# Performance work log

Measured on AMD Instinct MI355X. Metric: run time of the kernel, lower is better.

The kernel has to match this reference:

```python
import jax, jax.numpy as jnp
import numpy as np

M, N, T = 32, 32, 512
H1 = (M + N) * 10 * 8      # 5120
H2 = M * N * 4             # 4096
HID = 1000                 # GRU hidden (hardcoded in module)
EPS = 1e-12


def _l2norm(x):
    # torch.nn.functional.normalize: x / max(||x||_2, eps)
    return x / jnp.maximum(jnp.linalg.norm(x), EPS)


def setup_inputs() -> dict:
    key = jax.random.key(0)
    ks = jax.random.split(key, 16)
    rn = lambda k, shp, s: (jax.random.normal(k, shp, dtype=jnp.float32) * s)
    inp = {
        "y": rn(ks[0], (T, N), 1.0),
        "F": rn(ks[1], (M, M), 0.5 / np.sqrt(M)),   # stable dynamics
        "H": rn(ks[2], (N, M), 1.0 / np.sqrt(M)),
        "m1x0": rn(ks[3], (M,), 1.0),
        "h0": rn(ks[4], (HID,), 1.0),
        "W1": rn(ks[5], (H1, M + N), 1.0 / np.sqrt(M + N)),
        "b1": rn(ks[6], (H1,), 0.01),
        "Wih": rn(ks[7], (3 * HID, H1), 1.0 / np.sqrt(H1)),
        "bih": rn(ks[8], (3 * HID,), 0.01),
        "Whh": rn(ks[9], (3 * HID, HID), 1.0 / np.sqrt(HID)),
        "bhh": rn(ks[10], (3 * HID,), 0.01),
        "W2": rn(ks[11], (H2, HID), 1.0 / np.sqrt(HID)),
        "b2": rn(ks[12], (H2,), 0.01),
        "W3": rn(ks[13], (M * N, H2), 1.0 / np.sqrt(H2)),
        "b3": rn(ks[14], (M * N,), 0.01),
    }
    return inp


def reference(y, F, H, m1x0, h0, W1, b1, Wih, bih, Whh, bhh, W2, b2, W3, b3):
    m, n = F.shape[0], H.shape[0]

    def step(carry, yt):
        m1x_prior, m1x_post, h = carry
        # step_prior
        m1x_prev_prior = m1x_prior
        m1x_prior = F @ m1x_post              # [m]
        m1y = H @ m1x_prior                   # [n]
        # step_KGain_est: features
        dm1x_n = _l2norm(m1x_post - m1x_prev_prior)
        dm1y_n = _l2norm(yt - m1y)
        kin = jnp.concatenate([dm1y_n, dm1x_n])  # [n+m]
        # KGain_step: Linear+ReLU -> single-step GRU -> Linear+ReLU -> Linear
        x = jax.nn.relu(W1 @ kin + b1)        # [H1]
        gi = Wih @ x + bih                    # [3*HID]
        gh = Whh @ h + bhh
        ir, iz, ic = jnp.split(gi, 3)
        hr, hz, hc = jnp.split(gh, 3)
        r = jax.nn.sigmoid(ir + hr)
        z = jax.nn.sigmoid(iz + hz)
        c = jnp.tanh(ic + r * hc)
        h_new = (1.0 - z) * c + z * h         # GRU hidden [HID]
        l2 = jax.nn.relu(W2 @ h_new + b2)     # [H2]
        KG = (W3 @ l2 + b3).reshape(m, n)     # Kalman gain
        # KNet_step: innovation update
        m1x_post_new = m1x_prior + KG @ (yt - m1y)
        return (m1x_prior, m1x_post_new, h_new), m1x_post_new

    init = (m1x0, m1x0, h0)
    _, posts = jax.lax.scan(step, init, y)
    return posts  # [T, m]
```

## Files before the change

kernel.cpp:

```cpp
#include <hip/hip_runtime.h>
#include <cmath>

#define Mdim 32
#define Ndim 32
#define Tsteps 512
#define H1dim 5120
#define H2dim 4096
#define HIDdim 1000
#define NWG 256
#define NTHR 1024
#define POLLER 320

typedef unsigned int u32;
typedef unsigned short u16;

__device__ u16 g_w2b[H2dim * HIDdim];
__device__ u16 g_w3t[H2dim * Mdim * Ndim];

#define OFF_WIH 0
#define OFF_WHH 122880
#define OFF_UNION 146880
#define OFF_H9 157120
#define OFF_MISC 161640
#define SMEM_BYTES 162560

#define MI_POST 0
#define MI_PRIOR 32
#define MI_INNOV 96
#define MI_KIN 128
#define MI_GI 192
#define MI_GH 204

__device__ __forceinline__ u16 f2bf(float f) {
  u32 u = __float_as_uint(f);
  return (u16)((u + 0x7fffu + ((u >> 16) & 1u)) >> 16);
}
__device__ __forceinline__ float bflo(u32 u) { return __uint_as_float(u << 16); }
__device__ __forceinline__ float bfhi(u32 u) { return __uint_as_float(u & 0xffff0000u); }

__device__ __forceinline__ float dot4(float4 a, float4 b) {
  return a.x * b.x + a.y * b.y + a.z * b.z + a.w * b.w;
}
__device__ __forceinline__ float dot8_bb(uint4 a, uint4 b) {
  float s = 0.f;
  s = fmaf(bflo(a.x), bflo(b.x), s); s = fmaf(bfhi(a.x), bfhi(b.x), s);
  s = fmaf(bflo(a.y), bflo(b.y), s); s = fmaf(bfhi(a.y), bfhi(b.y), s);
  s = fmaf(bflo(a.z), bflo(b.z), s); s = fmaf(bfhi(a.z), bfhi(b.z), s);
  s = fmaf(bflo(a.w), bflo(b.w), s); s = fmaf(bfhi(a.w), bfhi(b.w), s);
  return s;
}
__device__ __forceinline__ float dot8_bf(uint4 a, const float* x8) {
  float s = 0.f;
  s = fmaf(bflo(a.x), x8[0], s); s = fmaf(bfhi(a.x), x8[1], s);
  s = fmaf(bflo(a.y), x8[2], s); s = fmaf(bfhi(a.y), x8[3], s);
  s = fmaf(bflo(a.z), x8[4], s); s = fmaf(bfhi(a.z), x8[5], s);
  s = fmaf(bflo(a.w), x8[6], s); s = fmaf(bfhi(a.w), x8[7], s);
  return s;
}

__device__ __forceinline__ float wave_reduce64(float v) {
#pragma unroll
  for (int off = 32; off >= 1; off >>= 1) v += __shfl_xor(v, off, 64);
  return v;
}
__device__ __forceinline__ float group16_reduce(float v) {
#pragma unroll
  for (int off = 8; off >= 1; off >>= 1) v += __shfl_xor(v, off, 64);
  return v;
}

__device__ __forceinline__ float4 ldg_cg4(const float* p) {
  float4 r;
  asm volatile("global_load_dwordx4 %0, %1, off sc0 sc1\n\ts_waitcnt vmcnt(0)"
               : "=v"(r) : "v"(p) : "memory");
  return r;
}
__device__ __forceinline__ uint4 ldg_cg4u(const void* p) {
  uint4 r;
  asm volatile("global_load_dwordx4 %0, %1, off sc0 sc1\n\ts_waitcnt vmcnt(0)"
               : "=v"(r) : "v"(p) : "memory");
  return r;
}
__device__ __forceinline__ void ldg2_cg4(const float* p0, const float* p1,
                                         float4& r0, float4& r1) {
  asm volatile("global_load_dwordx4 %0, %2, off sc0 sc1\n\t"
               "global_load_dwordx4 %1, %3, off sc0 sc1\n\t"
               "s_waitcnt vmcnt(0)"
               : "=&v"(r0), "=&v"(r1) : "v"(p0), "v"(p1) : "memory");
}
__device__ __forceinline__ void stg_cg1(float* p, float v) {
  asm volatile("global_store_dword %0, %1, off sc0 sc1" :: "v"(p), "v"(v) : "memory");
}
__device__ __forceinline__ void stg_cg_u16(u16* p, u16 v) {
  u32 vv = v;
  asm volatile("global_store_short %0, %1, off sc0 sc1" :: "v"(p), "v"(vv) : "memory");
}

__device__ __forceinline__ void gb_arrive(u32* bar) {
  asm volatile("s_waitcnt vmcnt(0)" ::: "memory");
  __syncthreads();
  if (threadIdx.x == POLLER) {
    u32 g = (u32)blockIdx.x & 15u;
    u32 a = __hip_atomic_fetch_add(bar + g * 16, 1u, __ATOMIC_RELAXED,
                                   __HIP_MEMORY_SCOPE_AGENT);
    if ((a & 15u) == 15u) {
      u32 b = __hip_atomic_fetch_add(bar + 256, 1u, __ATOMIC_RELAXED,
                                     __HIP_MEMORY_SCOPE_AGENT);
      if ((b & 15u) == 15u)
        __hip_atomic_fetch_add(bar + 320, 1u, __ATOMIC_RELAXED,
                               __HIP_MEMORY_SCOPE_AGENT);
    }
  }
}
__device__ __forceinline__ void gb_wait(u32* bar, u32 nb) {
  if (threadIdx.x == POLLER) {
    while (__hip_atomic_load(bar + 320, __ATOMIC_RELAXED,
                             __HIP_MEMORY_SCOPE_AGENT) < nb)
      __builtin_amdgcn_s_sleep(2);
  }
  __syncthreads();
}

__global__ void convert_w2(const float* __restrict__ W2) {
  int i = blockIdx.x * 1024 + threadIdx.x;
  if (i < H2dim * HIDdim) g_w2b[i] = f2bf(W2[i]);
}

__global__ void convert_w3t(const float* __restrict__ W3) {
  __shared__ float tile[32][33];
  int tr = blockIdx.x >> 7;
  int tc = blockIdx.x & 127;
  int r0 = tr * 32, c0 = tc * 32;
  int j = threadIdx.x & 31, i0 = threadIdx.x >> 5;
#pragma unroll
  for (int p = 0; p < 4; ++p) {
    int i = i0 + p * 8;
    tile[i][j] = W3[(size_t)(r0 + i) * H2dim + c0 + j];
  }
  __syncthreads();
#pragma unroll
  for (int p = 0; p < 4; ++p) {
    int i = i0 + p * 8;
    g_w3t[(size_t)(c0 + i) * 1024 + r0 + j] = f2bf(tile[j][i]);
  }
}

__global__ void __launch_bounds__(NTHR, 4)
knet_kernel(const float* __restrict__ y, const float* __restrict__ F,
            const float* __restrict__ Hm, const float* __restrict__ m1x0,
            const float* __restrict__ h0, const float* __restrict__ W1,
            const float* __restrict__ b1, const float* __restrict__ Wih,
            const float* __restrict__ bih, const float* __restrict__ Whh,
            const float* __restrict__ bhh, const float* __restrict__ b2,
            const float* __restrict__ b3, float* __restrict__ out,
            u32* bar, u16* xb, float* hbuf, float* dpart) {
  extern __shared__ char smem[];
  u16* s_wih = (u16*)(smem + OFF_WIH);
  u16* s_whh = (u16*)(smem + OFF_WHH);
  u16* s_x = (u16*)(smem + OFF_UNION);
  float4* s_red4 = (float4*)(smem + OFF_UNION);
  float* s_redf = (float*)(smem + OFF_UNION);
  float* s_pd = (float*)(smem + OFF_UNION);
  float* s_h9 = (float*)(smem + OFF_H9);
  float* s_m = (float*)(smem + OFF_MISC);
  float* s_post = s_m + MI_POST;
  float* s_prior = s_m + MI_PRIOR;
  float* s_innov = s_m + MI_INNOV;
  float* s_kin = s_m + MI_KIN;
  float* s_gi = s_m + MI_GI;
  float* s_gh = s_m + MI_GH;

  const int tid = threadIdx.x;
  const int w = tid >> 6;
  const int lane = tid & 63;
  const int wg = blockIdx.x;
  const int k0 = wg * 4;
  const bool gru_wg = (wg < 250);
  u32 nb = 0;

  if (gru_wg) {
#pragma unroll 1
    for (int r = 0; r < 12; ++r) {
      const float* src = Wih + (size_t)((r >> 2) * HIDdim + k0 + (r & 3)) * H1dim;
      u16* dst = s_wih + r * H1dim;
      for (int e = tid; e < H1dim; e += NTHR) dst[e] = f2bf(src[e]);
    }
#pragma unroll 1
    for (int r = 0; r < 12; ++r) {
      const float* src = Whh + (size_t)((r >> 2) * HIDdim + k0 + (r & 3)) * HIDdim;
      u16* dst = s_whh + r * HIDdim;
      for (int e = tid; e < HIDdim; e += NTHR) dst[e] = f2bf(src[e]);
    }
  }
  if (tid < 250) {
    float4 hv = ((const float4*)h0)[tid];
    int b0 = tid * 4;
    s_h9[((b0 + 0) >> 3) * 9 + ((b0 + 0) & 7)] = hv.x;
    s_h9[((b0 + 1) >> 3) * 9 + ((b0 + 1) & 7)] = hv.y;
    s_h9[((b0 + 2) >> 3) * 9 + ((b0 + 2) & 7)] = hv.z;
    s_h9[((b0 + 3) >> 3) * 9 + ((b0 + 3) & 7)] = hv.w;
  }
  __syncthreads();

  const int c2 = wg * 16 + w;
  const uint4* w2p = (const uint4*)(g_w2b + (size_t)c2 * HIDdim);
  uint4 wr0r = w2p[lane];
  uint4 wr1r = make_uint4(0u, 0u, 0u, 0u);
  if (lane < 61) wr1r = w2p[lane + 64];
  const uint4* w3p = (const uint4*)(g_w3t + (size_t)c2 * 1024);
  uint4 t0r = w3p[2 * lane];
  uint4 t1r = w3p[2 * lane + 1];
  const float b2c = b2[c2];
  float4 w1c = make_float4(0.f, 0.f, 0.f, 0.f);
  float b1c = 0.f;
  int w1row = 0;
  if (w < 5) {
    w1row = wg * 20 + w * 4 + (lane >> 4);
    w1c = ((const float4*)W1)[w1row * 16 + (lane & 15)];
    b1c = b1[w1row];
  }
  float prior = 0.f, bb = 0.f, yv = 0.f;
  if (w == 0 && lane < 32) {
    prior = m1x0[lane];
    yv = y[lane];
  }

  auto gh_compute = [&]() {
    int base = (w - 12) * 3;
#pragma unroll
    for (int rr = 0; rr < 3; ++rr) {
      int r = base + rr;
      const uint4* wr = (const uint4*)(s_whh + r * HIDdim);
      float acc = dot8_bf(wr[lane], s_h9 + lane * 9);
      if (lane < 61) acc += dot8_bf(wr[lane + 64], s_h9 + (lane + 64) * 9);
      acc = wave_reduce64(acc);
      if (lane == 0) s_gh[r] = acc + bhh[(r >> 2) * HIDdim + k0 + (r & 3)];
    }
  };
  if (gru_wg && w >= 12) gh_compute();

  for (int t = 0; t < Tsteps; ++t) {
    if (t > 0) {
      float4 a0, a1;
      ldg2_cg4(dpart + tid * 4, dpart + (tid + 1024) * 4, a0, a1);
      float4 s;
      s.x = a0.x + a1.x; s.y = a0.y + a1.y; s.z = a0.z + a1.z; s.w = a0.w + a1.w;
#pragma unroll
      for (int off = 8; off <= 32; off <<= 1) {
        s.x += __shfl_xor(s.x, off, 64);
        s.y += __shfl_xor(s.y, off, 64);
        s.z += __shfl_xor(s.z, off, 64);
        s.w += __shfl_xor(s.w, off, 64);
      }
      if (lane < 8) s_red4[w * 8 + lane] = s;
    }
    __syncthreads();
    if (w == 0) {
      float p = 0.f, inn = 0.f;
      float prev = prior;
      if (lane < 32) {
        if (t == 0) {
          p = m1x0[lane];
        } else {
          float dsum = 0.f;
#pragma unroll
          for (int ww = 0; ww < 16; ++ww) dsum += s_redf[ww * 32 + lane];
          p = prior + dsum + bb;
          if (wg == 0) out[(t - 1) * Mdim + lane] = p;
        }
        s_post[lane] = p;
      }
      asm volatile("" ::: "memory");
      if (lane < 32) {
        const float4* Fr = (const float4*)(F + lane * Mdim);
        const float4* pp = (const float4*)s_post;
        float s = 0.f;
#pragma unroll
        for (int j = 0; j < 8; ++j) s += dot4(Fr[j], pp[j]);
        prior = s;
        s_prior[lane] = s;
      }
      asm volatile("" ::: "memory");
      if (lane < 32) {
        const float4* Hr = (const float4*)(Hm + lane * Mdim);
        const float4* pp = (const float4*)s_prior;
        float s = 0.f;
#pragma unroll
        for (int j = 0; j < 8; ++j) s += dot4(Hr[j], pp[j]);
        inn = yv - s;
        s_innov[lane] = inn;
      }
      float vd = __shfl(p, lane & 31, 64) - __shfl(prev, lane & 31, 64);
      float v = (lane < 32) ? inn : vd;
      float sq = v * v;
#pragma unroll
      for (int off = 16; off >= 1; off >>= 1) sq += __shfl_xor(sq, off, 32);
      s_kin[lane] = v / fmaxf(sqrtf(sq), 1e-12f);
    }
    __syncthreads();
    if (w < 5) {
      float s = dot4(w1c, ((const float4*)s_kin)[lane & 15]);
      s = group16_reduce(s);
      if ((lane & 15) == 0) stg_cg_u16(xb + w1row, f2bf(fmaxf(s + b1c, 0.f)));
    }
    ++nb;
    gb_arrive(bar);
    gb_wait(bar, nb);

    if (gru_wg) {
      if (tid < 640) ((uint4*)s_x)[tid] = ldg_cg4u((const char*)xb + tid * 16);
      __syncthreads();
      if (w < 12) {
        const uint4* wr = (const uint4*)(s_wih + w * H1dim);
        const uint4* xr = (const uint4*)s_x;
        float acc = 0.f;
#pragma unroll
        for (int i = 0; i < 10; ++i) {
          int j = lane + 64 * i;
          acc += dot8_bb(wr[j], xr[j]);
        }
        acc = wave_reduce64(acc);
        if (lane == 0) s_gi[w] = acc + bih[(w >> 2) * HIDdim + k0 + (w & 3)];
      }
      __syncthreads();
      if (tid < 4) {
        int k = k0 + tid;
        float hold = s_h9[(k >> 3) * 9 + (k & 7)];
        float ir = s_gi[tid], iz = s_gi[4 + tid], ic = s_gi[8 + tid];
        float r = 1.f / (1.f + expf(-(ir + s_gh[tid])));
        float z = 1.f / (1.f + expf(-(iz + s_gh[4 + tid])));
        float c_ = tanhf(ic + r * s_gh[8 + tid]);
        stg_cg1(hbuf + k, (1.f - z) * c_ + z * hold);
      }
    }
    ++nb;
    gb_arrive(bar);
    float u;
    {
      const float* iv = s_innov + 16 * (lane & 1);
      u = dot8_bf(t0r, iv) + dot8_bf(t1r, iv + 8);
      u += __shfl_xor(u, 1, 64);
    }
    gb_wait(bar, nb);

    if (tid < 250) {
      float4 hv = ldg_cg4(hbuf + tid * 4);
      int b0 = tid * 4;
      s_h9[((b0 + 0) >> 3) * 9 + ((b0 + 0) & 7)] = hv.x;
      s_h9[((b0 + 1) >> 3) * 9 + ((b0 + 1) & 7)] = hv.y;
      s_h9[((b0 + 2) >> 3) * 9 + ((b0 + 2) & 7)] = hv.z;
      s_h9[((b0 + 3) >> 3) * 9 + ((b0 + 3) & 7)] = hv.w;
    }
    __syncthreads();
    {
      float acc = dot8_bf(wr0r, s_h9 + lane * 9);
      if (lane < 61) acc += dot8_bf(wr1r, s_h9 + (lane + 64) * 9);
      acc = wave_reduce64(acc);
      float l2c = fmaxf(acc + b2c, 0.f);
      if ((lane & 1) == 0) s_pd[w * 32 + (lane >> 1)] = l2c * u;
    }
    __syncthreads();
    if (tid < 32) {
      float pdv = 0.f;
#pragma unroll
      for (int ww = 0; ww < 16; ++ww) pdv += s_pd[ww * 32 + tid];
      stg_cg1(dpart + wg * 32 + tid, pdv);
    }
    ++nb;
    gb_arrive(bar);
    if (gru_wg && w >= 12) gh_compute();
    if (w == 0 && lane < 32) {
      int tn = (t + 1 < Tsteps) ? t + 1 : Tsteps - 1;
      yv = y[tn * Ndim + lane];
      float b = 0.f;
#pragma unroll 8
      for (int j = 0; j < 32; ++j) b = fmaf(b3[lane * 32 + j], s_innov[j], b);
      bb = b;
    }
    gb_wait(bar, nb);
  }

  if (wg == 0) {
    float4 a0, a1;
    ldg2_cg4(dpart + tid * 4, dpart + (tid + 1024) * 4, a0, a1);
    float4 s;
    s.x = a0.x + a1.x; s.y = a0.y + a1.y; s.z = a0.z + a1.z; s.w = a0.w + a1.w;
#pragma unroll
    for (int off = 8; off <= 32; off <<= 1) {
      s.x += __shfl_xor(s.x, off, 64);
      s.y += __shfl_xor(s.y, off, 64);
      s.z += __shfl_xor(s.z, off, 64);
      s.w += __shfl_xor(s.w, off, 64);
    }
    if (lane < 8) s_red4[w * 8 + lane] = s;
    __syncthreads();
    if (w == 0 && lane < 32) {
      float d = 0.f;
#pragma unroll
      for (int ww = 0; ww < 16; ++ww) d += s_redf[ww * 32 + lane];
      out[(Tsteps - 1) * Mdim + lane] = prior + d + bb;
    }
  }
}

extern "C" void kernel_launch(void* const* d_in, const int* in_sizes, int n_in,
                              void* d_out, int out_size, void* d_ws, size_t ws_size,
                              hipStream_t stream) {
  const float* y    = (const float*)d_in[0];
  const float* F    = (const float*)d_in[1];
  const float* Hm   = (const float*)d_in[2];
  const float* m1x0 = (const float*)d_in[3];
  const float* h0   = (const float*)d_in[4];
  const float* W1   = (const float*)d_in[5];
  const float* b1   = (const float*)d_in[6];
  const float* Wih  = (const float*)d_in[7];
  const float* bih  = (const float*)d_in[8];
  const float* Whh  = (const float*)d_in[9];
  const float* bhh  = (const float*)d_in[10];
  const float* W2   = (const float*)d_in[11];
  const float* b2   = (const float*)d_in[12];
  const float* W3   = (const float*)d_in[13];
  const float* b3   = (const float*)d_in[14];
  float* out = (float*)d_out;

  u32* bar   = (u32*)d_ws;
  u16* xb    = (u16*)((char*)d_ws + 4096);
  float* hbuf  = (float*)((char*)d_ws + 14336);
  float* dpart = (float*)((char*)d_ws + 18432);

  convert_w2<<<4000, 1024, 0, stream>>>(W2);
  convert_w3t<<<4096, 256, 0, stream>>>(W3);
  hipMemsetAsync(d_ws, 0, 4096, stream);
  hipFuncSetAttribute((const void*)knet_kernel,
                      hipFuncAttributeMaxDynamicSharedMemorySize, SMEM_BYTES);
  void* args[] = {&y, &F, &Hm, &m1x0, &h0, &W1, &b1, &Wih, &bih, &Whh, &bhh,
                  &b2, &b3, &out, &bar, &xb, &hbuf, &dpart};
  hipLaunchCooperativeKernel((const void*)knet_kernel, dim3(NWG), dim3(NTHR),
                             args, SMEM_BYTES, stream);
}
```

Baseline: 7.007 ms.

## Flatten grid barrier to two levels and stream weights from global each step

The grid barrier drops its middle counter level. Each group of 16 workgroups now bumps the final counter directly, and waiters compare against nb*16. Separately, the W2/W3/W1 weight fragments held in registers for the whole run are replaced by per-step loads from global (L2-resident bf16) memory, and the launch-bounds occupancy hint is relaxed. This aims to shorten barrier latency and cut register pressure, at the cost of more contention on one atomic and extra global loads on the critical path every step.

```diff
diff --git a/kernel.cpp b/kernel.cpp
--- a/kernel.cpp
+++ b/kernel.cpp
@@ -103,19 +103,16 @@
     u32 g = (u32)blockIdx.x & 15u;
     u32 a = __hip_atomic_fetch_add(bar + g * 16, 1u, __ATOMIC_RELAXED,
                                    __HIP_MEMORY_SCOPE_AGENT);
-    if ((a & 15u) == 15u) {
-      u32 b = __hip_atomic_fetch_add(bar + 256, 1u, __ATOMIC_RELAXED,
-                                     __HIP_MEMORY_SCOPE_AGENT);
-      if ((b & 15u) == 15u)
-        __hip_atomic_fetch_add(bar + 320, 1u, __ATOMIC_RELAXED,
-                               __HIP_MEMORY_SCOPE_AGENT);
-    }
+    if ((a & 15u) == 15u)
+      __hip_atomic_fetch_add(bar + 320, 1u, __ATOMIC_RELAXED,
+                             __HIP_MEMORY_SCOPE_AGENT);
   }
 }
 __device__ __forceinline__ void gb_wait(u32* bar, u32 nb) {
   if (threadIdx.x == POLLER) {
+    const u32 target = nb * 16u;
     while (__hip_atomic_load(bar + 320, __ATOMIC_RELAXED,
-                             __HIP_MEMORY_SCOPE_AGENT) < nb)
+                             __HIP_MEMORY_SCOPE_AGENT) < target)
       __builtin_amdgcn_s_sleep(2);
   }
   __syncthreads();
@@ -145,7 +142,7 @@
   }
 }
 
-__global__ void __launch_bounds__(NTHR, 4)
+__global__ void __launch_bounds__(NTHR)
 knet_kernel(const float* __restrict__ y, const float* __restrict__ F,
             const float* __restrict__ Hm, const float* __restrict__ m1x0,
             const float* __restrict__ h0, const float* __restrict__ W1,
@@ -203,22 +200,7 @@
   __syncthreads();
 
   const int c2 = wg * 16 + w;
-  const uint4* w2p = (const uint4*)(g_w2b + (size_t)c2 * HIDdim);
-  uint4 wr0r = w2p[lane];
-  uint4 wr1r = make_uint4(0u, 0u, 0u, 0u);
-  if (lane < 61) wr1r = w2p[lane + 64];
-  const uint4* w3p = (const uint4*)(g_w3t + (size_t)c2 * 1024);
-  uint4 t0r = w3p[2 * lane];
-  uint4 t1r = w3p[2 * lane + 1];
-  const float b2c = b2[c2];
-  float4 w1c = make_float4(0.f, 0.f, 0.f, 0.f);
-  float b1c = 0.f;
-  int w1row = 0;
-  if (w < 5) {
-    w1row = wg * 20 + w * 4 + (lane >> 4);
-    w1c = ((const float4*)W1)[w1row * 16 + (lane & 15)];
-    b1c = b1[w1row];
-  }
+  const int w1row = wg * 20 + w * 4 + (lane >> 4);
   float prior = 0.f, bb = 0.f, yv = 0.f;
   if (w == 0 && lane < 32) {
     prior = m1x0[lane];
@@ -299,9 +281,10 @@
     }
     __syncthreads();
     if (w < 5) {
-      float s = dot4(w1c, ((const float4*)s_kin)[lane & 15]);
+      float s = dot4(((const float4*)W1)[w1row * 16 + (lane & 15)],
+                     ((const float4*)s_kin)[lane & 15]);
       s = group16_reduce(s);
-      if ((lane & 15) == 0) stg_cg_u16(xb + w1row, f2bf(fmaxf(s + b1c, 0.f)));
+      if ((lane & 15) == 0) stg_cg_u16(xb + w1row, f2bf(fmaxf(s + b1[w1row], 0.f)));
     }
     ++nb;
     gb_arrive(bar);
@@ -336,10 +319,16 @@
     ++nb;
     gb_arrive(bar);
     float u;
+    uint4 w2a, w2b_;
     {
+      const uint4* tr3 = (const uint4*)(g_w3t + (size_t)c2 * 1024);
+      uint4 t0 = tr3[2 * lane], t1 = tr3[2 * lane + 1];
       const float* iv = s_innov + 16 * (lane & 1);
-      u = dot8_bf(t0r, iv) + dot8_bf(t1r, iv + 8);
+      u = dot8_bf(t0, iv) + dot8_bf(t1, iv + 8);
       u += __shfl_xor(u, 1, 64);
+      const uint4* w2p = (const uint4*)(g_w2b + (size_t)c2 * HIDdim);
+      w2a = w2p[lane];
+      w2b_ = (lane < 61) ? w2p[lane + 64] : make_uint4(0u, 0u, 0u, 0u);
     }
     gb_wait(bar, nb);
 
@@ -353,10 +342,10 @@
     }
     __syncthreads();
     {
-      float acc = dot8_bf(wr0r, s_h9 + lane * 9);
-      if (lane < 61) acc += dot8_bf(wr1r, s_h9 + (lane + 64) * 9);
+      float acc = dot8_bf(w2a, s_h9 + lane * 9);
+      if (lane < 61) acc += dot8_bf(w2b_, s_h9 + (lane + 64) * 9);
       acc = wave_reduce64(acc);
-      float l2c = fmaxf(acc + b2c, 0.f);
+      float l2c = fmaxf(acc + b2[c2], 0.f);
       if ((lane & 1) == 0) s_pd[w * 32 + (lane >> 1)] = l2c * u;
     }
     __syncthreads();
```

After: 7.458 ms. +6.4%, slower.
